# Kernel optimization log

Hardware: AMD Instinct MI355X
Metric: run time of the kernel (lower is better)

## Reference

```python
import jax, jax.numpy as jnp
import numpy as np

N = 50000      # nodes
E = 800000     # edges
D_IN = 128
D_H = 256
D_OUT = 128
EPS = 1e-5
SLOPE = 0.01   # LeakyReLU negative_slope


def setup_inputs() -> dict:
    key = jax.random.key(0)
    ks = jax.random.split(key, 24)
    inp = {}
    inp["x"] = jax.random.normal(ks[0], (N, D_IN), dtype=jnp.float32)
    inp["edge_index"] = jax.random.randint(ks[1], (2, E), 0, N, dtype=jnp.int32)
    dims = [(D_IN, D_H), (D_H, D_H), (D_H, D_H), (D_H, D_OUT)]
    for i, (di, do) in enumerate(dims, start=1):
        inp[f"W{i}"] = jax.random.normal(ks[4 * i - 2], (di, do), dtype=jnp.float32) / np.float32(np.sqrt(di))
        inp[f"b{i}"] = jnp.zeros((do,), dtype=jnp.float32)
        inp[f"g{i}"] = 1.0 + 0.1 * jax.random.normal(ks[4 * i - 1], (do,), dtype=jnp.float32)   # BN gamma
        inp[f"be{i}"] = 0.1 * jax.random.normal(ks[4 * i], (do,), dtype=jnp.float32)            # BN beta
    inp["ln_g"] = 1.0 + 0.1 * jax.random.normal(ks[18], (D_OUT,), dtype=jnp.float32)
    inp["ln_b"] = 0.1 * jax.random.normal(ks[19], (D_OUT,), dtype=jnp.float32)
    return inp


def _gcn_conv(x, W, b, src, dst, nisq):
    # PyG GCNConv: linear first, then sym-normalized aggregation with self-loops.
    xl = x @ W                                   # [N, do]
    coef = (nisq[src] * nisq[dst])[:, None]      # [E, 1]
    msg = xl[src] * coef                         # [E, do] gather
    agg = jax.ops.segment_sum(msg, dst, num_segments=N)  # scatter-add
    # self-loop contribution: deg^{-1/2}_i * deg^{-1/2}_i * xl_i
    return agg + xl * (nisq * nisq)[:, None] + b


def _bn(x, g, b):
    # BatchNorm1d, training-mode batch statistics (biased variance)
    m = jnp.mean(x, axis=0)
    v = jnp.var(x, axis=0)
    return (x - m) * jax.lax.rsqrt(v + EPS) * g + b


def _lrelu(x):
    return jnp.where(x >= 0, x, SLOPE * x)


def _layer_norm(x, g, b):
    m = jnp.mean(x, axis=-1, keepdims=True)
    v = jnp.var(x, axis=-1, keepdims=True)
    return (x - m) * jax.lax.rsqrt(v + EPS) * g + b


def reference(x, edge_index, W1, b1, g1, be1, W2, b2, g2, be2, W3, b3, g3, be3, W4, b4, g4, be4, ln_g, ln_b):
    src = edge_index[0]
    dst = edge_index[1]
    # degrees with self-loops (computed once, shared by all 4 convs)
    deg = jax.ops.segment_sum(jnp.ones((E,), dtype=x.dtype), dst, num_segments=N) + 1.0
    nisq = jax.lax.rsqrt(deg)  # deg >= 1 so safe

    identity = x  # input_dim == output_dim -> residual_fc is Identity
    h = _lrelu(_bn(_gcn_conv(x, W1, b1, src, dst, nisq), g1, be1))   # dropout = identity (eval)
    h = _lrelu(_bn(_gcn_conv(h, W2, b2, src, dst, nisq), g2, be2))
    h = _lrelu(_bn(_gcn_conv(h, W3, b3, src, dst, nisq), g3, be3))
    h = _gcn_conv(h, W4, b4, src, dst, nisq)
    h = h + identity
    return _layer_norm(_bn(h, g4, be4), ln_g, ln_b)
```

## Files before the change

kernel.cpp:

```cpp
#include <hip/hip_runtime.h>

#define N_NODES 50000
#define N_EDGES 800000
#define EPS_C 1e-5f
#define SLOPE_C 0.01f

typedef __attribute__((ext_vector_type(8))) short short8v;
typedef __attribute__((ext_vector_type(4))) float f32x4;

__device__ __forceinline__ unsigned short f2bf(float f) {
  unsigned u = __float_as_uint(f);
  u += 0x7fffu + ((u >> 16) & 1u);
  return (unsigned short)(u >> 16);
}
__device__ __forceinline__ unsigned packbf(float a, float b) {
  return (unsigned)f2bf(a) | ((unsigned)f2bf(b) << 16);
}
__device__ __forceinline__ float bflo(unsigned u) { return __uint_as_float(u << 16); }
__device__ __forceinline__ float bfhi(unsigned u) { return __uint_as_float(u & 0xffff0000u); }

__global__ void wcast_kernel(const float* __restrict__ W, unsigned short* __restrict__ Wt,
                             int total, int mshift, int mmask, int K) {
  const int idx = blockIdx.x * 256 + threadIdx.x;
  if (idx >= total) return;
  const int k = idx >> mshift;
  const int m = idx & mmask;
  Wt[(size_t)m * K + k] = f2bf(W[idx]);
}

template <int MODE>
__global__ __launch_bounds__(256) void gemm_mfma_kernel(
    const unsigned short* __restrict__ A, const unsigned short* __restrict__ Wt,
    const float* __restrict__ bias, unsigned short* __restrict__ Yb,
    float* __restrict__ colsum, float* __restrict__ colsumsq,
    int Nrows, int K, int M) {
  __shared__ __align__(16) unsigned short As[128][72];
  __shared__ __align__(16) unsigned short Bs[64][72];
  __shared__ float sred[2][64][8];
  const int tid = threadIdx.x;
  const int lane = tid & 63;
  const int wave = tid >> 6;
  const int wr = wave >> 1, wc = wave & 1;
  const int row0 = blockIdx.x * 128;
  const int col0 = blockIdx.y * 64;
  const int l15 = lane & 15;
  const int lhi = lane >> 4;
  f32x4 acc[4][2];
#pragma unroll
  for (int i = 0; i < 4; ++i)
#pragma unroll
    for (int j = 0; j < 2; ++j) acc[i][j] = (f32x4){0.f, 0.f, 0.f, 0.f};

  for (int k0 = 0; k0 < K; k0 += 64) {
#pragma unroll
    for (int c = 0; c < 4; ++c) {
      const int id = tid + c * 256;
      const int r = id >> 3;
      const int ck = (id & 7) * 8;
      short8v v = {};
      const int grow = row0 + r;
      if (grow < Nrows)
        v = *reinterpret_cast<const short8v*>(&A[(size_t)grow * K + k0 + ck]);
      *reinterpret_cast<short8v*>(&As[r][ck]) = v;
    }
#pragma unroll
    for (int c = 0; c < 2; ++c) {
      const int id = tid + c * 256;
      const int r = id >> 3;
      const int ck = (id & 7) * 8;
      const short8v v =
          *reinterpret_cast<const short8v*>(&Wt[(size_t)(col0 + r) * K + k0 + ck]);
      *reinterpret_cast<short8v*>(&Bs[r][ck]) = v;
    }
    __syncthreads();
    short8v bfr[2][2];
#pragma unroll
    for (int nr = 0; nr < 2; ++nr)
#pragma unroll
      for (int h = 0; h < 2; ++h)
        bfr[nr][h] = *reinterpret_cast<const short8v*>(
            &Bs[wc * 32 + nr * 16 + l15][h * 32 + lhi * 8]);
#pragma unroll
    for (int mr = 0; mr < 4; ++mr) {
#pragma unroll
      for (int h = 0; h < 2; ++h) {
        const short8v af = *reinterpret_cast<const short8v*>(
            &As[wr * 64 + mr * 16 + l15][h * 32 + lhi * 8]);
#pragma unroll
        for (int nr = 0; nr < 2; ++nr)
          acc[mr][nr] = __builtin_amdgcn_mfma_f32_16x16x32_bf16(
              af, bfr[nr][h], acc[mr][nr], 0, 0, 0);
      }
    }
    __syncthreads();
  }
  float bcol[2] = {0.f, 0.f};
  if constexpr (MODE == 1) {
#pragma unroll
    for (int nr = 0; nr < 2; ++nr) bcol[nr] = bias[col0 + wc * 32 + nr * 16 + l15];
  }
  float s_c[2] = {0.f, 0.f}, q_c[2] = {0.f, 0.f};
#pragma unroll
  for (int mr = 0; mr < 4; ++mr) {
#pragma unroll
    for (int r = 0; r < 4; ++r) {
      const int grow = row0 + wr * 64 + mr * 16 + lhi * 4 + r;
      const bool ok = (grow < Nrows);
#pragma unroll
      for (int nr = 0; nr < 2; ++nr) {
        const int gcol = col0 + wc * 32 + nr * 16 + l15;
        float v = acc[mr][nr][r] + bcol[nr];
        if (ok) {
          Yb[(size_t)grow * M + gcol] = f2bf(v);
          if constexpr (MODE == 1) {
            s_c[nr] += v;
            q_c[nr] += v * v;
          }
        }
      }
    }
  }
  if constexpr (MODE == 1) {
    const int contrib = wr * 4 + lhi;
#pragma unroll
    for (int nr = 0; nr < 2; ++nr) {
      const int cl = wc * 32 + nr * 16 + l15;
      sred[0][cl][contrib] = s_c[nr];
      sred[1][cl][contrib] = q_c[nr];
    }
    __syncthreads();
    if (tid < 128) {
      const int which = tid >> 6;
      const int cl = tid & 63;
      float acc8 = 0.f;
#pragma unroll
      for (int k = 0; k < 8; ++k) acc8 += sred[which][cl][k];
      float* dstp = which ? colsumsq : colsum;
      atomicAdd(&dstp[col0 + cl], acc8);
    }
  }
}

__global__ void hist_kernel(const int* __restrict__ dst, int* __restrict__ hist, int E) {
  const int e = blockIdx.x * 256 + threadIdx.x;
  if (e < E) atomicAdd(&hist[dst[e]], 1);
}

__global__ void nisq_kernel(const int* __restrict__ hist, float* __restrict__ nisq, int n) {
  const int i = blockIdx.x * 256 + threadIdx.x;
  if (i < n) nisq[i] = rsqrtf((float)hist[i] + 1.0f);
}

__global__ __launch_bounds__(1024) void scan1_kernel(
    const int* __restrict__ hist, int* __restrict__ off, int* __restrict__ partial, int n) {
  __shared__ int tmp[1024];
  const int tid = threadIdx.x;
  const int i = blockIdx.x * 1024 + tid;
  const int v = (i < n) ? hist[i] : 0;
  tmp[tid] = v;
  __syncthreads();
  int x = v;
  for (int o = 1; o < 1024; o <<= 1) {
    const int y = (tid >= o) ? tmp[tid - o] : 0;
    __syncthreads();
    x += y;
    tmp[tid] = x;
    __syncthreads();
  }
  if (i < n) off[i] = x - v;
  if (tid == 1023) partial[blockIdx.x] = x;
}

__global__ __launch_bounds__(64) void scan2_kernel(
    const int* __restrict__ partial, int* __restrict__ partialoff,
    int* __restrict__ offN, int nb) {
  const int tid = threadIdx.x;
  const int v = (tid < nb) ? partial[tid] : 0;
  int x = v;
  for (int o = 1; o < 64; o <<= 1) {
    const int y = __shfl_up(x, o, 64);
    if (tid >= o) x += y;
  }
  if (tid < nb) partialoff[tid] = x - v;
  if (tid == 63) *offN = x;
}

__global__ void scan3_kernel(int* __restrict__ off, int* __restrict__ cursor,
                             const int* __restrict__ partialoff, int n) {
  const int i = blockIdx.x * 256 + threadIdx.x;
  if (i < n) {
    const int o = off[i] + partialoff[i >> 10];
    off[i] = o;
    cursor[i] = o;
  }
}

__global__ void scatter_kernel(const int* __restrict__ src, const int* __restrict__ dst,
                               int* __restrict__ cursor, int* __restrict__ esorted, int E) {
  const int e = blockIdx.x * 256 + threadIdx.x;
  if (e < E) {
    const int p = atomicAdd(&cursor[dst[e]], 1);
    esorted[p] = src[e];
  }
}

__global__ void scale_cast_kernel(const float* __restrict__ x,
                                  const float* __restrict__ nisq,
                                  unsigned short* __restrict__ xs) {
  const int idx = blockIdx.x * 256 + threadIdx.x;
  if (idx >= N_NODES * 32) return;
  const int row = idx >> 5;
  const int c = (idx & 31) * 4;
  const float s = nisq[row];
  const float4 v = *reinterpret_cast<const float4*>(&x[(size_t)row * 128 + c]);
  ushort4 o;
  o.x = f2bf(v.x * s); o.y = f2bf(v.y * s);
  o.z = f2bf(v.z * s); o.w = f2bf(v.w * s);
  *reinterpret_cast<ushort4*>(&xs[(size_t)row * 128 + c]) = o;
}

template <int DO, bool ADD_BIAS, bool HAS_RES, bool OUT_BF16>
__global__ __launch_bounds__(256) void aggregate3_kernel(
    const unsigned short* __restrict__ Y, const int* __restrict__ segoff,
    const int* __restrict__ esorted, const float* __restrict__ nisq,
    const float* __restrict__ bias, const float* __restrict__ resid,
    void* __restrict__ Tv) {
  constexpr int V2 = DO / 32;
  const int wave = threadIdx.x >> 6;
  const int lane = threadIdx.x & 63;
  const int half = lane >> 5;
  const int l31 = lane & 31;
  const int n = blockIdx.x * 4 + wave;
  if (n >= N_NODES) return;
  const int colbase = l31 * V2;
  float a0[V2], a1[V2];
#pragma unroll
  for (int i = 0; i < V2; ++i) { a0[i] = 0.f; a1[i] = 0.f; }
  const int s = segoff[n];
  const int e = segoff[n + 1];
  auto addrow = [&](float* a, int rid) {
    const unsigned short* yr = Y + (size_t)rid * DO + colbase;
    if constexpr (V2 == 8) {
      const uint4 v = *reinterpret_cast<const uint4*>(yr);
      a[0] += bflo(v.x); a[1] += bfhi(v.x);
      a[2] += bflo(v.y); a[3] += bfhi(v.y);
      a[4] += bflo(v.z); a[5] += bfhi(v.z);
      a[6] += bflo(v.w); a[7] += bfhi(v.w);
    } else {
      const uint2 v = *reinterpret_cast<const uint2*>(yr);
      a[0] += bflo(v.x); a[1] += bfhi(v.x);
      a[2] += bflo(v.y); a[3] += bfhi(v.y);
    }
  };
  int j = s + half;
  for (; j + 2 < e; j += 4) {
    const int i0 = esorted[j];
    const int i1 = esorted[j + 2];
    addrow(a0, i0);
    addrow(a1, i1);
  }
  if (j < e) addrow(a0, esorted[j]);
  if (half == 0) addrow(a1, n);
  const float sc = nisq[n];
  float vals[V2];
#pragma unroll
  for (int i = 0; i < V2; ++i) {
    float t = a0[i] + a1[i];
    t += __shfl_xor(t, 32, 64);
    t *= sc;
    if (half == 0) {
      if (ADD_BIAS) t += bias[colbase + i];
      if (HAS_RES) t += resid[(size_t)n * DO + colbase + i];
    }
    vals[i] = t;
  }
  if (half == 0) {
    if constexpr (OUT_BF16) {
      unsigned short* tr = (unsigned short*)Tv + (size_t)n * DO + colbase;
      if constexpr (V2 == 8) {
        uint4 o;
        o.x = packbf(vals[0], vals[1]); o.y = packbf(vals[2], vals[3]);
        o.z = packbf(vals[4], vals[5]); o.w = packbf(vals[6], vals[7]);
        *reinterpret_cast<uint4*>(tr) = o;
      } else {
        uint2 o;
        o.x = packbf(vals[0], vals[1]); o.y = packbf(vals[2], vals[3]);
        *reinterpret_cast<uint2*>(tr) = o;
      }
    } else {
      float* tr = (float*)Tv + (size_t)n * DO + colbase;
      if constexpr (V2 == 8) {
        float4 o0 = {vals[0], vals[1], vals[2], vals[3]};
        float4 o1 = {vals[4], vals[5], vals[6], vals[7]};
        *reinterpret_cast<float4*>(tr) = o0;
        *reinterpret_cast<float4*>(tr + 4) = o1;
      } else {
        float4 o = {vals[0], vals[1], vals[2], vals[3]};
        *reinterpret_cast<float4*>(tr) = o;
      }
    }
  }
}

__global__ void stats_kernel(const float* __restrict__ T, float* __restrict__ colsum,
                             float* __restrict__ colsumsq, int n, int rowsPerBlock) {
  const int c = threadIdx.x;
  const int DO = blockDim.x;
  const int r0 = blockIdx.x * rowsPerBlock;
  int r1 = r0 + rowsPerBlock;
  if (r1 > n) r1 = n;
  float s = 0.f, q = 0.f;
  for (int r = r0; r < r1; ++r) {
    const float v = T[(size_t)r * DO + c];
    s += v;
    q += v * v;
  }
  atomicAdd(&colsum[c], s);
  atomicAdd(&colsumsq[c], q);
}

__global__ void bn_lrelu_nisq_kernel(const unsigned short* __restrict__ Tb,
                                     const float* __restrict__ colsum,
                                     const float* __restrict__ colsumsq,
                                     const float* __restrict__ g, const float* __restrict__ be,
                                     const float* __restrict__ nisq,
                                     unsigned short* __restrict__ outb,
                                     size_t total8, float invN) {
  const size_t idx = (size_t)blockIdx.x * 256 + threadIdx.x;
  if (idx >= total8) return;
  const unsigned c = ((unsigned)idx & 31u) * 8;
  const int row = (int)(idx >> 5);
  const float sc = nisq[row];
  uint4 v = *reinterpret_cast<const uint4*>(&Tb[idx * 8]);
  float z[8] = {bflo(v.x), bfhi(v.x), bflo(v.y), bfhi(v.y),
                bflo(v.z), bfhi(v.z), bflo(v.w), bfhi(v.w)};
  const float4 cs0 = *reinterpret_cast<const float4*>(&colsum[c]);
  const float4 cs1 = *reinterpret_cast<const float4*>(&colsum[c + 4]);
  const float4 cq0 = *reinterpret_cast<const float4*>(&colsumsq[c]);
  const float4 cq1 = *reinterpret_cast<const float4*>(&colsumsq[c + 4]);
  const float4 gv0 = *reinterpret_cast<const float4*>(&g[c]);
  const float4 gv1 = *reinterpret_cast<const float4*>(&g[c + 4]);
  const float4 bv0 = *reinterpret_cast<const float4*>(&be[c]);
  const float4 bv1 = *reinterpret_cast<const float4*>(&be[c + 4]);
  const float css[8] = {cs0.x, cs0.y, cs0.z, cs0.w, cs1.x, cs1.y, cs1.z, cs1.w};
  const float cqq[8] = {cq0.x, cq0.y, cq0.z, cq0.w, cq1.x, cq1.y, cq1.z, cq1.w};
  const float ggg[8] = {gv0.x, gv0.y, gv0.z, gv0.w, gv1.x, gv1.y, gv1.z, gv1.w};
  const float bbb[8] = {bv0.x, bv0.y, bv0.z, bv0.w, bv1.x, bv1.y, bv1.z, bv1.w};
#pragma unroll
  for (int k = 0; k < 8; ++k) {
    const float m = css[k] * invN;
    const float rs = rsqrtf(cqq[k] * invN - m * m + EPS_C);
    float zz = (z[k] - m) * rs * ggg[k] + bbb[k];
    zz = (zz >= 0.f) ? zz : SLOPE_C * zz;
    z[k] = zz * sc;
  }
  v.x = packbf(z[0], z[1]); v.y = packbf(z[2], z[3]);
  v.z = packbf(z[4], z[5]); v.w = packbf(z[6], z[7]);
  *reinterpret_cast<uint4*>(&outb[idx * 8]) = v;
}

__global__ __launch_bounds__(256) void bn_ln_kernel(
    const float* __restrict__ T, const float* __restrict__ colsum,
    const float* __restrict__ colsumsq, const float* __restrict__ g,
    const float* __restrict__ be, const float* __restrict__ lng,
    const float* __restrict__ lnb, float* __restrict__ out, float invN) {
  const int wave = threadIdx.x >> 6;
  const int lane = threadIdx.x & 63;
  const int n = blockIdx.x * 4 + wave;
  if (n >= N_NODES) return;
  const int c = lane * 2;
  const float2 t = *reinterpret_cast<const float2*>(&T[(size_t)n * 128 + c]);
  float z[2];
#pragma unroll
  for (int k = 0; k < 2; ++k) {
    const float m = colsum[c + k] * invN;
    const float v = colsumsq[c + k] * invN - m * m;
    const float tv = (k == 0) ? t.x : t.y;
    z[k] = (tv - m) * rsqrtf(v + EPS_C) * g[c + k] + be[c + k];
  }
  float s = z[0] + z[1];
  float q = z[0] * z[0] + z[1] * z[1];
  for (int o = 32; o > 0; o >>= 1) {
    s += __shfl_xor(s, o, 64);
    q += __shfl_xor(q, o, 64);
  }
  const float mean = s * (1.f / 128.f);
  const float var = q * (1.f / 128.f) - mean * mean;
  const float rs = rsqrtf(var + EPS_C);
  float2 o2;
  o2.x = (z[0] - mean) * rs * lng[c] + lnb[c];
  o2.y = (z[1] - mean) * rs * lng[c + 1] + lnb[c + 1];
  *reinterpret_cast<float2*>(&out[(size_t)n * 128 + c]) = o2;
}

extern "C" void kernel_launch(void* const* d_in, const int* in_sizes, int n_in,
                              void* d_out, int out_size, void* d_ws, size_t ws_size,
                              hipStream_t stream) {
  const float* x = (const float*)d_in[0];
  const int* ei = (const int*)d_in[1];
  const int* srcp = ei;
  const int* dstp = ei + N_EDGES;
  const float* W1 = (const float*)d_in[2];
  const float* b1 = (const float*)d_in[3];
  const float* g1 = (const float*)d_in[4];
  const float* be1 = (const float*)d_in[5];
  const float* W2 = (const float*)d_in[6];
  const float* b2 = (const float*)d_in[7];
  const float* g2 = (const float*)d_in[8];
  const float* be2 = (const float*)d_in[9];
  const float* W3 = (const float*)d_in[10];
  const float* b3 = (const float*)d_in[11];
  const float* g3 = (const float*)d_in[12];
  const float* be3 = (const float*)d_in[13];
  const float* W4 = (const float*)d_in[14];
  const float* b4 = (const float*)d_in[15];
  const float* g4 = (const float*)d_in[16];
  const float* be4 = (const float*)d_in[17];
  const float* lng = (const float*)d_in[18];
  const float* lnb = (const float*)d_in[19];
  float* out = (float*)d_out;

  char* ws = (char*)d_ws;
  size_t off_b = 0;
  auto alloc = [&](size_t bytes) -> void* {
    void* p = (void*)(ws + off_b);
    off_b += (bytes + 255) & ~(size_t)255;
    return p;
  };
  int* hist = (int*)alloc((size_t)N_NODES * 4);
  int* segoff = (int*)alloc((size_t)(N_NODES + 1) * 4);
  int* cursor = (int*)alloc((size_t)N_NODES * 4);
  float* nisq = (float*)alloc((size_t)N_NODES * 4);
  int* esorted = (int*)alloc((size_t)N_EDGES * 4);
  int* partial = (int*)alloc(64 * 4);
  int* partialoff = (int*)alloc(64 * 4);
  float* colsum = (float*)alloc(256 * 4);
  float* colsumsq = (float*)alloc(256 * 4);
  unsigned short* Wt1 = (unsigned short*)alloc((size_t)256 * 128 * 2);
  unsigned short* Wt2 = (unsigned short*)alloc((size_t)256 * 256 * 2);
  unsigned short* Wt3 = (unsigned short*)alloc((size_t)256 * 256 * 2);
  unsigned short* Wt4 = (unsigned short*)alloc((size_t)128 * 256 * 2);
  unsigned short* tblA = (unsigned short*)alloc((size_t)N_NODES * 256 * 2);
  unsigned short* tblB = (unsigned short*)alloc((size_t)N_NODES * 256 * 2);
  unsigned short* S = (unsigned short*)alloc((size_t)N_NODES * 256 * 2);
  unsigned short* Tb = (unsigned short*)alloc((size_t)N_NODES * 256 * 2);
  float* Tf = (float*)alloc((size_t)N_NODES * 128 * 4);

  const float invN = 1.0f / (float)N_NODES;
  const int egrid = (N_EDGES + 255) / 256;
  const int ngrid = (N_NODES + 255) / 256;
  const int aggrid = (N_NODES + 3) / 4;
  const int statgrid = (N_NODES + 127) / 128;
  const int nb = (N_NODES + 1023) / 1024;
  const dim3 mgrid256((N_NODES + 127) / 128, 4);
  const dim3 mgrid128((N_NODES + 127) / 128, 2);
  const unsigned bngrid = (unsigned)(((size_t)N_NODES * 32 + 255) / 256);

  hipMemsetAsync(hist, 0, (size_t)N_NODES * 4, stream);
  hist_kernel<<<egrid, 256, 0, stream>>>(dstp, hist, N_EDGES);
  nisq_kernel<<<ngrid, 256, 0, stream>>>(hist, nisq, N_NODES);
  scan1_kernel<<<nb, 1024, 0, stream>>>(hist, segoff, partial, N_NODES);
  scan2_kernel<<<1, 64, 0, stream>>>(partial, partialoff, &segoff[N_NODES], nb);
  scan3_kernel<<<ngrid, 256, 0, stream>>>(segoff, cursor, partialoff, N_NODES);
  scatter_kernel<<<egrid, 256, 0, stream>>>(srcp, dstp, cursor, esorted, N_EDGES);

  wcast_kernel<<<(128 * 256 + 255) / 256, 256, 0, stream>>>(W1, Wt1, 128 * 256, 8, 255, 128);
  wcast_kernel<<<(256 * 256 + 255) / 256, 256, 0, stream>>>(W2, Wt2, 256 * 256, 8, 255, 256);
  wcast_kernel<<<(256 * 256 + 255) / 256, 256, 0, stream>>>(W3, Wt3, 256 * 256, 8, 255, 256);
  wcast_kernel<<<(256 * 128 + 255) / 256, 256, 0, stream>>>(W4, Wt4, 256 * 128, 7, 127, 256);

  scale_cast_kernel<<<(N_NODES * 32 + 255) / 256, 256, 0, stream>>>(x, nisq, tblA);
  aggregate3_kernel<128, false, false, true><<<aggrid, 256, 0, stream>>>(
      tblA, segoff, esorted, nisq, nullptr, nullptr, S);
  hipMemsetAsync(colsum, 0, 2048, stream);
  gemm_mfma_kernel<1><<<mgrid256, 256, 0, stream>>>(S, Wt1, b1, Tb, colsum, colsumsq,
                                                    N_NODES, 128, 256);
  bn_lrelu_nisq_kernel<<<bngrid, 256, 0, stream>>>(Tb, colsum, colsumsq, g1, be1, nisq,
                                                   tblB, (size_t)N_NODES * 32, invN);

  aggregate3_kernel<256, false, false, true><<<aggrid, 256, 0, stream>>>(
      tblB, segoff, esorted, nisq, nullptr, nullptr, S);
  hipMemsetAsync(colsum, 0, 2048, stream);
  gemm_mfma_kernel<1><<<mgrid256, 256, 0, stream>>>(S, Wt2, b2, Tb, colsum, colsumsq,
                                                    N_NODES, 256, 256);
  bn_lrelu_nisq_kernel<<<bngrid, 256, 0, stream>>>(Tb, colsum, colsumsq, g2, be2, nisq,
                                                   tblA, (size_t)N_NODES * 32, invN);

  aggregate3_kernel<256, false, false, true><<<aggrid, 256, 0, stream>>>(
      tblA, segoff, esorted, nisq, nullptr, nullptr, S);
  hipMemsetAsync(colsum, 0, 2048, stream);
  gemm_mfma_kernel<1><<<mgrid256, 256, 0, stream>>>(S, Wt3, b3, Tb, colsum, colsumsq,
                                                    N_NODES, 256, 256);
  bn_lrelu_nisq_kernel<<<bngrid, 256, 0, stream>>>(Tb, colsum, colsumsq, g3, be3, nisq,
                                                   tblB, (size_t)N_NODES * 32, invN);

  gemm_mfma_kernel<0><<<mgrid128, 256, 0, stream>>>(tblB, Wt4, nullptr, S, nullptr, nullptr,
                                                    N_NODES, 256, 128);
  aggregate3_kernel<128, true, true, false><<<aggrid, 256, 0, stream>>>(
      S, segoff, esorted, nisq, b4, x, Tf);
  hipMemsetAsync(colsum, 0, 2048, stream);
  stats_kernel<<<statgrid, 128, 0, stream>>>(Tf, colsum, colsumsq, N_NODES, 128);
  bn_ln_kernel<<<aggrid, 256, 0, stream>>>(Tf, colsum, colsumsq, g4, be4, lng, lnb, out, invN);
}
```

Measured before the change: 555.8 us.

## Merge small setup kernels, consolidate memsets, and unroll aggregation gathers by four

Folds the four weight-cast launches into one 2D-grid kernel and computes nisq inside the first scan kernel, dropping a separate launch. It gives each layer its own column-stat buffers so a single memset zeroes them all up front, removing four per-layer memsets. The aggregation loop now issues four independent row gathers per iteration instead of two, exposing more memory-level parallelism at some register cost. Several unrelated launch-overhead trims plus a loop unroll are bundled together.

```diff
diff --git a/kernel.cpp b/kernel.cpp
--- a/kernel.cpp
+++ b/kernel.cpp
@@ -19,9 +19,21 @@
 __device__ __forceinline__ float bflo(unsigned u) { return __uint_as_float(u << 16); }
 __device__ __forceinline__ float bfhi(unsigned u) { return __uint_as_float(u & 0xffff0000u); }
 
-__global__ void wcast_kernel(const float* __restrict__ W, unsigned short* __restrict__ Wt,
-                             int total, int mshift, int mmask, int K) {
+__global__ void wcast_all_kernel(const float* __restrict__ W1, const float* __restrict__ W2,
+                                 const float* __restrict__ W3, const float* __restrict__ W4,
+                                 unsigned short* __restrict__ Wt1, unsigned short* __restrict__ Wt2,
+                                 unsigned short* __restrict__ Wt3, unsigned short* __restrict__ Wt4) {
+  const int y = blockIdx.y;
   const int idx = blockIdx.x * 256 + threadIdx.x;
+  const float* W;
+  unsigned short* Wt;
+  int K, mshift, mmask, total;
+  switch (y) {
+    case 0: W = W1; Wt = Wt1; K = 128; mshift = 8; mmask = 255; total = 32768; break;
+    case 1: W = W2; Wt = Wt2; K = 256; mshift = 8; mmask = 255; total = 65536; break;
+    case 2: W = W3; Wt = Wt3; K = 256; mshift = 8; mmask = 255; total = 65536; break;
+    default: W = W4; Wt = Wt4; K = 256; mshift = 7; mmask = 127; total = 32768; break;
+  }
   if (idx >= total) return;
   const int k = idx >> mshift;
   const int m = idx & mmask;
@@ -146,13 +158,9 @@
   if (e < E) atomicAdd(&hist[dst[e]], 1);
 }
 
-__global__ void nisq_kernel(const int* __restrict__ hist, float* __restrict__ nisq, int n) {
-  const int i = blockIdx.x * 256 + threadIdx.x;
-  if (i < n) nisq[i] = rsqrtf((float)hist[i] + 1.0f);
-}
-
 __global__ __launch_bounds__(1024) void scan1_kernel(
-    const int* __restrict__ hist, int* __restrict__ off, int* __restrict__ partial, int n) {
+    const int* __restrict__ hist, int* __restrict__ off, int* __restrict__ partial,
+    float* __restrict__ nisq, int n) {
   __shared__ int tmp[1024];
   const int tid = threadIdx.x;
   const int i = blockIdx.x * 1024 + tid;
@@ -167,7 +175,10 @@
     tmp[tid] = x;
     __syncthreads();
   }
-  if (i < n) off[i] = x - v;
+  if (i < n) {
+    off[i] = x - v;
+    nisq[i] = rsqrtf((float)v + 1.0f);
+  }
   if (tid == 1023) partial[blockIdx.x] = x;
 }
 
@@ -220,7 +231,7 @@
 }
 
 template <int DO, bool ADD_BIAS, bool HAS_RES, bool OUT_BF16>
-__global__ __launch_bounds__(256) void aggregate3_kernel(
+__global__ __launch_bounds__(256) void aggregate4_kernel(
     const unsigned short* __restrict__ Y, const int* __restrict__ segoff,
     const int* __restrict__ esorted, const float* __restrict__ nisq,
     const float* __restrict__ bias, const float* __restrict__ resid,
@@ -233,34 +244,57 @@
   const int n = blockIdx.x * 4 + wave;
   if (n >= N_NODES) return;
   const int colbase = l31 * V2;
+  const unsigned short* Yc = Y + colbase;
   float a0[V2], a1[V2];
 #pragma unroll
   for (int i = 0; i < V2; ++i) { a0[i] = 0.f; a1[i] = 0.f; }
   const int s = segoff[n];
   const int e = segoff[n + 1];
-  auto addrow = [&](float* a, int rid) {
-    const unsigned short* yr = Y + (size_t)rid * DO + colbase;
-    if constexpr (V2 == 8) {
-      const uint4 v = *reinterpret_cast<const uint4*>(yr);
+
+  if constexpr (V2 == 8) {
+    auto acc8 = [&](float* a, const uint4 v) {
       a[0] += bflo(v.x); a[1] += bfhi(v.x);
       a[2] += bflo(v.y); a[3] += bfhi(v.y);
       a[4] += bflo(v.z); a[5] += bfhi(v.z);
       a[6] += bflo(v.w); a[7] += bfhi(v.w);
-    } else {
-      const uint2 v = *reinterpret_cast<const uint2*>(yr);
+    };
+    int j = s + half;
+    for (; j + 6 < e; j += 8) {
+      const int i0 = esorted[j];
+      const int i1 = esorted[j + 2];
+      const int i2 = esorted[j + 4];
+      const int i3 = esorted[j + 6];
+      const uint4 v0 = *reinterpret_cast<const uint4*>(Yc + (size_t)i0 * DO);
+      const uint4 v1 = *reinterpret_cast<const uint4*>(Yc + (size_t)i1 * DO);
+      const uint4 v2 = *reinterpret_cast<const uint4*>(Yc + (size_t)i2 * DO);
+      const uint4 v3 = *reinterpret_cast<const uint4*>(Yc + (size_t)i3 * DO);
+      acc8(a0, v0); acc8(a1, v1); acc8(a0, v2); acc8(a1, v3);
+    }
+    for (; j < e; j += 2)
+      acc8(a0, *reinterpret_cast<const uint4*>(Yc + (size_t)esorted[j] * DO));
+    if (half == 0) acc8(a1, *reinterpret_cast<const uint4*>(Yc + (size_t)n * DO));
+  } else {
+    auto acc4 = [&](float* a, const uint2 v) {
       a[0] += bflo(v.x); a[1] += bfhi(v.x);
       a[2] += bflo(v.y); a[3] += bfhi(v.y);
-    }
-  };
-  int j = s + half;
-  for (; j + 2 < e; j += 4) {
-    const int i0 = esorted[j];
-    const int i1 = esorted[j + 2];
-    addrow(a0, i0);
-    addrow(a1, i1);
-  }
-  if (j < e) addrow(a0, esorted[j]);
-  if (half == 0) addrow(a1, n);
+    };
+    int j = s + half;
+    for (; j + 6 < e; j += 8) {
+      const int i0 = esorted[j];
+      const int i1 = esorted[j + 2];
+      const int i2 = esorted[j + 4];
+      const int i3 = esorted[j + 6];
+      const uint2 v0 = *reinterpret_cast<const uint2*>(Yc + (size_t)i0 * DO);
+      const uint2 v1 = *reinterpret_cast<const uint2*>(Yc + (size_t)i1 * DO);
+      const uint2 v2 = *reinterpret_cast<const uint2*>(Yc + (size_t)i2 * DO);
+      const uint2 v3 = *reinterpret_cast<const uint2*>(Yc + (size_t)i3 * DO);
+      acc4(a0, v0); acc4(a1, v1); acc4(a0, v2); acc4(a1, v3);
+    }
+    for (; j < e; j += 2)
+      acc4(a0, *reinterpret_cast<const uint2*>(Yc + (size_t)esorted[j] * DO));
+    if (half == 0) acc4(a1, *reinterpret_cast<const uint2*>(Yc + (size_t)n * DO));
+  }
+
   const float sc = nisq[n];
   float vals[V2];
 #pragma unroll
@@ -428,14 +462,21 @@
     return p;
   };
   int* hist = (int*)alloc((size_t)N_NODES * 4);
+  float* cs1 = (float*)alloc(256 * 4);
+  float* cq1 = (float*)alloc(256 * 4);
+  float* cs2 = (float*)alloc(256 * 4);
+  float* cq2 = (float*)alloc(256 * 4);
+  float* cs3 = (float*)alloc(256 * 4);
+  float* cq3 = (float*)alloc(256 * 4);
+  float* cs4 = (float*)alloc(256 * 4);
+  float* cq4 = (float*)alloc(256 * 4);
+  const size_t zero_bytes = off_b;
   int* segoff = (int*)alloc((size_t)(N_NODES + 1) * 4);
   int* cursor = (int*)alloc((size_t)N_NODES * 4);
   float* nisq = (float*)alloc((size_t)N_NODES * 4);
   int* esorted = (int*)alloc((size_t)N_EDGES * 4);
   int* partial = (int*)alloc(64 * 4);
   int* partialoff = (int*)alloc(64 * 4);
-  float* colsum = (float*)alloc(256 * 4);
-  float* colsumsq = (float*)alloc(256 * 4);
   unsigned short* Wt1 = (unsigned short*)alloc((size_t)256 * 128 * 2);
   unsigned short* Wt2 = (unsigned short*)alloc((size_t)256 * 256 * 2);
   unsigned short* Wt3 = (unsigned short*)alloc((size_t)256 * 256 * 2);
@@ -456,49 +497,42 @@
   const dim3 mgrid128((N_NODES + 127) / 128, 2);
   const unsigned bngrid = (unsigned)(((size_t)N_NODES * 32 + 255) / 256);
 
-  hipMemsetAsync(hist, 0, (size_t)N_NODES * 4, stream);
+  hipMemsetAsync(hist, 0, zero_bytes, stream);
+
   hist_kernel<<<egrid, 256, 0, stream>>>(dstp, hist, N_EDGES);
-  nisq_kernel<<<ngrid, 256, 0, stream>>>(hist, nisq, N_NODES);
-  scan1_kernel<<<nb, 1024, 0, stream>>>(hist, segoff, partial, N_NODES);
+  scan1_kernel<<<nb, 1024, 0, stream>>>(hist, segoff, partial, nisq, N_NODES);
   scan2_kernel<<<1, 64, 0, stream>>>(partial, partialoff, &segoff[N_NODES], nb);
   scan3_kernel<<<ngrid, 256, 0, stream>>>(segoff, cursor, partialoff, N_NODES);
   scatter_kernel<<<egrid, 256, 0, stream>>>(srcp, dstp, cursor, esorted, N_EDGES);
 
-  wcast_kernel<<<(128 * 256 + 255) / 256, 256, 0, stream>>>(W1, Wt1, 128 * 256, 8, 255, 128);
-  wcast_kernel<<<(256 * 256 + 255) / 256, 256, 0, stream>>>(W2, Wt2, 256 * 256, 8, 255, 256);
-  wcast_kernel<<<(256 * 256 + 255) / 256, 256, 0, stream>>>(W3, Wt3, 256 * 256, 8, 255, 256);
-  wcast_kernel<<<(256 * 128 + 255) / 256, 256, 0, stream>>>(W4, Wt4, 256 * 128, 7, 127, 256);
+  wcast_all_kernel<<<dim3(256, 4), 256, 0, stream>>>(W1, W2, W3, W4, Wt1, Wt2, Wt3, Wt4);
 
   scale_cast_kernel<<<(N_NODES * 32 + 255) / 256, 256, 0, stream>>>(x, nisq, tblA);
-  aggregate3_kernel<128, false, false, true><<<aggrid, 256, 0, stream>>>(
+  aggregate4_kernel<128, false, false, true><<<aggrid, 256, 0, stream>>>(
       tblA, segoff, esorted, nisq, nullptr, nullptr, S);
-  hipMemsetAsync(colsum, 0, 2048, stream);
-  gemm_mfma_kernel<1><<<mgrid256, 256, 0, stream>>>(S, Wt1, b1, Tb, colsum, colsumsq,
+  gemm_mfma_kernel<1><<<mgrid256, 256, 0, stream>>>(S, Wt1, b1, Tb, cs1, cq1,
                                                     N_NODES, 128, 256);
-  bn_lrelu_nisq_kernel<<<bngrid, 256, 0, stream>>>(Tb, colsum, colsumsq, g1, be1, nisq,
+  bn_lrelu_nisq_kernel<<<bngrid, 256, 0, stream>>>(Tb, cs1, cq1, g1, be1, nisq,
                                                    tblB, (size_t)N_NODES * 32, invN);
 
-  aggregate3_kernel<256, false, false, true><<<aggrid, 256, 0, stream>>>(
+  aggregate4_kernel<256, false, false, true><<<aggrid, 256, 0, stream>>>(
       tblB, segoff, esorted, nisq, nullptr, nullptr, S);
-  hipMemsetAsync(colsum, 0, 2048, stream);
-  gemm_mfma_kernel<1><<<mgrid256, 256, 0, stream>>>(S, Wt2, b2, Tb, colsum, colsumsq,
+  gemm_mfma_kernel<1><<<mgrid256, 256, 0, stream>>>(S, Wt2, b2, Tb, cs2, cq2,
                                                     N_NODES, 256, 256);
-  bn_lrelu_nisq_kernel<<<bngrid, 256, 0, stream>>>(Tb, colsum, colsumsq, g2, be2, nisq,
+  bn_lrelu_nisq_kernel<<<bngrid, 256, 0, stream>>>(Tb, cs2, cq2, g2, be2, nisq,
                                                    tblA, (size_t)N_NODES * 32, invN);
 
-  aggregate3_kernel<256, false, false, true><<<aggrid, 256, 0, stream>>>(
+  aggregate4_kernel<256, false, false, true><<<aggrid, 256, 0, stream>>>(
       tblA, segoff, esorted, nisq, nullptr, nullptr, S);
-  hipMemsetAsync(colsum, 0, 2048, stream);
-  gemm_mfma_kernel<1><<<mgrid256, 256, 0, stream>>>(S, Wt3, b3, Tb, colsum, colsumsq,
+  gemm_mfma_kernel<1><<<mgrid256, 256, 0, stream>>>(S, Wt3, b3, Tb, cs3, cq3,
                                                     N_NODES, 256, 256);
-  bn_lrelu_nisq_kernel<<<bngrid, 256, 0, stream>>>(Tb, colsum, colsumsq, g3, be3, nisq,
+  bn_lrelu_nisq_kernel<<<bngrid, 256, 0, stream>>>(Tb, cs3, cq3, g3, be3, nisq,
                                                    tblB, (size_t)N_NODES * 32, invN);
 
   gemm_mfma_kernel<0><<<mgrid128, 256, 0, stream>>>(tblB, Wt4, nullptr, S, nullptr, nullptr,
                                                     N_NODES, 256, 128);
-  aggregate3_kernel<128, true, true, false><<<aggrid, 256, 0, stream>>>(
+  aggregate4_kernel<128, true, true, false><<<aggrid, 256, 0, stream>>>(
       S, segoff, esorted, nisq, b4, x, Tf);
-  hipMemsetAsync(colsum, 0, 2048, stream);
-  stats_kernel<<<statgrid, 128, 0, stream>>>(Tf, colsum, colsumsq, N_NODES, 128);
-  bn_ln_kernel<<<aggrid, 256, 0, stream>>>(Tf, colsum, colsumsq, g4, be4, lng, lnb, out, invN);
-}
+  stats_kernel<<<statgrid, 128, 0, stream>>>(Tf, cs4, cq4, N_NODES, 128);
+  bn_ln_kernel<<<aggrid, 256, 0, stream>>>(Tf, cs4, cq4, g4, be4, lng, lnb, out, invN);
+}
```

New measurement: 531.6 us. -4.4%, faster.
